# Performance work log

Hardware: AMD Instinct MI355X
Metric: run time of the kernel (lower is better)

## Reference

```python
import jax, jax.numpy as jnp
import numpy as np

B, T, C, U = 256, 512, 256, 64  # batch, time, classes (incl. blank), label length
BLANK = C - 1                   # keras ctc_batch_cost: blank is last class
S = 2 * U + 1                   # extended label length (blanks interleaved)
NEG = -1e30                     # safe log-zero for fp32
EPS = 1e-7                      # keras.backend.epsilon()


def setup_inputs() -> dict:
    key = jax.random.key(0)
    k1, k2 = jax.random.split(key)
    # y_pred are softmax probabilities over time, as fed to ctc_batch_cost
    y_pred = jax.nn.softmax(jax.random.normal(k1, (B, T, C), dtype=jnp.float32), axis=-1)
    # labels exclude the blank index (values in [0, C-2]); all U positions valid
    y_true = jax.random.randint(k2, (B, U), 0, C - 1, dtype=jnp.int32)
    return {"y_true": y_true, "y_pred": y_pred}


def _ctc_loss(y_pred, y_true):
    # keras ctc_batch_cost computes loss on log(y_pred + eps)
    log_probs = jnp.log(y_pred + EPS)                      # [B, T, C]
    # extended label sequence: blank, l1, blank, l2, ..., blank
    ext = jnp.full((B, S), BLANK, dtype=y_true.dtype).at[:, 1::2].set(y_true)
    # gather per-state emission log-probs: lp_ext[b,t,s] = log_probs[b,t,ext[b,s]]
    lp_ext = jnp.take_along_axis(log_probs, ext[:, None, :].astype(jnp.int32), axis=2)  # [B,T,S]
    # skip transition (s-2 -> s) allowed iff ext[s] != blank and ext[s] != ext[s-2]
    ext_m2 = jnp.pad(ext[:, :-2], ((0, 0), (2, 0)), constant_values=-1)
    skip_ok = (ext != BLANK) & (ext != ext_m2)             # [B, S]

    # alpha_0: can start in state 0 (blank) or state 1 (first label)
    alpha0 = (jnp.full((B, S), NEG, dtype=jnp.float32)
              .at[:, 0].set(lp_ext[:, 0, 0])
              .at[:, 1].set(lp_ext[:, 0, 1]))

    def step(alpha, lp_t):
        a1 = jnp.pad(alpha[:, :-1], ((0, 0), (1, 0)), constant_values=NEG)
        a2 = jnp.pad(alpha[:, :-2], ((0, 0), (2, 0)), constant_values=NEG)
        a2 = jnp.where(skip_ok, a2, NEG)
        alpha = jnp.logaddexp(jnp.logaddexp(alpha, a1), a2) + lp_t
        return alpha, None

    lp_time_major = jnp.swapaxes(lp_ext, 0, 1)             # [T, B, S]
    alpha, _ = jax.lax.scan(step, alpha0, lp_time_major[1:])
    # terminate in last blank or last label
    loss = -jnp.logaddexp(alpha[:, -1], alpha[:, -2])      # [B]
    return loss[:, None]                                   # [B, 1] like ctc_batch_cost


def reference(y_true, y_pred):
    return _ctc_loss(y_pred, y_true)
```

## Files before the change

### kernel.cpp

```cpp
#include <hip/hip_runtime.h>


constexpr int B = 256, T = 512, C = 256, U = 64;
constexpr int CH = 16;
constexpr int NBUF = 4;
#define EPSF 1e-7f

__device__ __forceinline__ float dpp_wave_shr1(float x) {
    return __int_as_float(__builtin_amdgcn_update_dpp(
        0, __float_as_int(x), 0x138, 0xf, 0xf, true));
}

#define DPPMAX(ctrl)                                                      \
    {                                                                     \
        float x_ = __int_as_float(__builtin_amdgcn_update_dpp(            \
            0, __float_as_int(m_), (ctrl), 0xf, 0xf, true));              \
        m_ = fmaxf(m_, x_);                                               \
    }

#define RESCALE()                                                         \
    {                                                                     \
        float m_ = fmaxf(fmaxf(a_even, a_odd), a_top);                    \
        DPPMAX(0x111) DPPMAX(0x112) DPPMAX(0x114) DPPMAX(0x118)           \
        DPPMAX(0x142) DPPMAX(0x143)                                       \
        const float mx_ = __int_as_float(                                 \
            __builtin_amdgcn_readlane(__float_as_int(m_), 63));           \
        int e_ = (__float_as_int(mx_) >> 23) & 0xff;                      \
        int k_ = 187 - e_;                                                \
        k_ = k_ > 127 ? 127 : k_;                                         \
        const float s_ = __int_as_float((k_ + 127) << 23);                \
        a_even *= s_; a_odd *= s_; a_top *= s_;                           \
        esum += k_;                                                       \
    }

#define STAGE(cc)                                                          \
    {                                                                      \
        const int cs_ = (cc);                                              \
        float* lbase_ = &rows[cs_ % NBUF][0][0];                           \
        _Pragma("unroll")                                                  \
        for (int i = 0; i < CH; ++i) {                                     \
            int t = 1 + cs_ * CH + i;                                      \
            t = t < T ? t : T - 1;                                         \
            const float* g_ = rowp + (size_t)t * C + (lane << 2);          \
            __builtin_amdgcn_global_load_lds(                              \
                (const __attribute__((address_space(1))) void*)g_,         \
                (__attribute__((address_space(3))) void*)(lbase_ + i * C), \
                16, 0, 0);                                                 \
        }                                                                  \
    }

#define DSR(dst, addr, OS)                                                 \
    asm volatile("ds_read_b32 %0, %1 offset:" OS                           \
                 : "=v"(dst) : "v"(addr));

#define LDS_ISSUE(cc)                                                      \
    {                                                                      \
        const int cr_ = (cc);                                              \
        float(*row_)[C] = rows[cr_ % NBUF];                                \
        const unsigned labA_ = (unsigned)(size_t)                          \
            (__attribute__((address_space(3))) void*)&row_[0][label];      \
        const unsigned blkA_ = (unsigned)(size_t)                          \
            (__attribute__((address_space(3))) void*)&row_[0][C - 1];      \
        DSR(lab[0],  labA_, "0")     DSR(lab[1],  labA_, "1024")           \
        DSR(lab[2],  labA_, "2048")  DSR(lab[3],  labA_, "3072")           \
        DSR(lab[4],  labA_, "4096")  DSR(lab[5],  labA_, "5120")           \
        DSR(lab[6],  labA_, "6144")  DSR(lab[7],  labA_, "7168")           \
        DSR(lab[8],  labA_, "8192")  DSR(lab[9],  labA_, "9216")           \
        DSR(lab[10], labA_, "10240") DSR(lab[11], labA_, "11264")          \
        DSR(lab[12], labA_, "12288") DSR(lab[13], labA_, "13312")          \
        DSR(lab[14], labA_, "14336") DSR(lab[15], labA_, "15360")          \
        DSR(blk[0],  blkA_, "0")     DSR(blk[1],  blkA_, "1024")           \
        DSR(blk[2],  blkA_, "2048")  DSR(blk[3],  blkA_, "3072")           \
        DSR(blk[4],  blkA_, "4096")  DSR(blk[5],  blkA_, "5120")           \
        DSR(blk[6],  blkA_, "6144")  DSR(blk[7],  blkA_, "7168")           \
        DSR(blk[8],  blkA_, "8192")  DSR(blk[9],  blkA_, "9216")           \
        DSR(blk[10], blkA_, "10240") DSR(blk[11], blkA_, "11264")          \
        DSR(blk[12], blkA_, "12288") DSR(blk[13], blkA_, "13312")          \
        DSR(blk[14], blkA_, "14336") DSR(blk[15], blkA_, "15360")          \
    }

#define LGKM_FENCE()                                                       \
    asm volatile("s_waitcnt lgkmcnt(0)" ::: "memory");                     \
    __builtin_amdgcn_sched_barrier(0);

#define COMP_CHUNK(NSTEPS)                                                 \
    {                                                                      \
        _Pragma("unroll")                                                  \
        for (int i = 0; i < (NSTEPS); ++i) {                               \
            const float pb = blk[i] + EPSF;                                \
            const float pl = lab[i] + EPSF;                                \
            const float po = dpp_wave_shr1(a_odd);                         \
            const float skp = skip_ok ? po : 0.f;                          \
            const float ne = (a_even + po) * pb;                           \
            const float no = (a_odd + a_even + skp) * pl;                  \
            const float nt = (a_top + a_odd) * pb;                         \
            a_even = ne; a_odd = no; a_top = nt;                           \
            if (((1 + i) & 7) == 0) RESCALE();                             \
        }                                                                  \
    }

__global__ __launch_bounds__(64) void ctc_kernel(const int* __restrict__ y_true,
                                                 const float* __restrict__ y_pred,
                                                 float* __restrict__ out) {
    __shared__ float rows[NBUF][CH][C];
    const int b = blockIdx.x;
    const int lane = threadIdx.x;
    const int label = y_true[b * U + lane];
    const int label_prev = __shfl_up(label, 1);
    const bool skip_ok = (lane > 0) && (label != label_prev);
    const float* __restrict__ rowp = y_pred + (size_t)b * (T * C);

    float a_even, a_odd, a_top;
    {
        const float pb = rowp[C - 1] + EPSF;
        const float pl = rowp[label] + EPSF;
        a_even = (lane == 0) ? pb : 0.f;
        a_odd  = (lane == 0) ? pl : 0.f;
        a_top  = 0.f;
    }
    int esum = 0;

    STAGE(0);
    STAGE(1);
    STAGE(2);

    float lab[CH], blk[CH];

    for (int c = 0; c < 30; ++c) {
        asm volatile("s_waitcnt vmcnt(32)" ::: "memory");
        __builtin_amdgcn_sched_barrier(0);
        LDS_ISSUE(c);
        __builtin_amdgcn_sched_barrier(0);
        if (c <= 28) STAGE(c + 3);
        LGKM_FENCE();
        COMP_CHUNK(CH);
    }

    {
        asm volatile("s_waitcnt vmcnt(16)" ::: "memory");
        __builtin_amdgcn_sched_barrier(0);
        LDS_ISSUE(30);
        LGKM_FENCE();
        COMP_CHUNK(CH);
    }
    {
        asm volatile("s_waitcnt vmcnt(0)" ::: "memory");
        __builtin_amdgcn_sched_barrier(0);
        LDS_ISSUE(31);
        LGKM_FENCE();
        COMP_CHUNK(CH - 1);
    }

    if (lane == 63)
        out[b] = -logf(a_top + a_odd) + (float)esum * 0.69314718055994531f;
}

extern "C" void kernel_launch(void* const* d_in, const int* in_sizes, int n_in,
                              void* d_out, int out_size, void* d_ws, size_t ws_size,
                              hipStream_t stream) {
    const int* y_true   = (const int*)d_in[0];
    const float* y_pred = (const float*)d_in[1];
    float* out = (float*)d_out;
    hipLaunchKernelGGL(ctc_kernel, dim3(B), dim3(64), 0, stream,
                       y_true, y_pred, out);
}
```

Measured before the change: 193.3 us.

## Split prefetch across four waves with one compute wave and block barriers

The block grows from one wave to four. Each wave now issues global-to-LDS loads for a quarter of the rows in every chunk, while wave 0 alone runs the CTC recurrence. Workgroup barriers, combined with vmcnt waits, coordinate buffer readiness between the waves. The goal is to take load-issue overhead off the serial compute wave. The cost is a barrier per chunk and extra waves competing for issue slots.

```diff
diff --git a/kernel.cpp b/kernel.cpp
--- a/kernel.cpp
+++ b/kernel.cpp
@@ -33,12 +33,13 @@
         esum += k_;                                                       \
     }
 
-#define STAGE(cc)                                                          \
+#define STAGE_W(cc)                                                        \
     {                                                                      \
         const int cs_ = (cc);                                              \
         float* lbase_ = &rows[cs_ % NBUF][0][0];                           \
         _Pragma("unroll")                                                  \
-        for (int i = 0; i < CH; ++i) {                                     \
+        for (int j = 0; j < 4; ++j) {                                      \
+            const int i = rbase + j;                                       \
             int t = 1 + cs_ * CH + i;                                      \
             t = t < T ? t : T - 1;                                         \
             const float* g_ = rowp + (size_t)t * C + (lane << 2);          \
@@ -99,60 +100,68 @@
         }                                                                  \
     }
 
-__global__ __launch_bounds__(64) void ctc_kernel(const int* __restrict__ y_true,
-                                                 const float* __restrict__ y_pred,
-                                                 float* __restrict__ out) {
+__global__ __launch_bounds__(256) void ctc_kernel(const int* __restrict__ y_true,
+                                                  const float* __restrict__ y_pred,
+                                                  float* __restrict__ out) {
     __shared__ float rows[NBUF][CH][C];
     const int b = blockIdx.x;
-    const int lane = threadIdx.x;
-    const int label = y_true[b * U + lane];
-    const int label_prev = __shfl_up(label, 1);
-    const bool skip_ok = (lane > 0) && (label != label_prev);
+    const int tid = threadIdx.x;
+    const int lane = tid & 63;
+    const int wid = tid >> 6;
+    const int rbase = wid << 2;
     const float* __restrict__ rowp = y_pred + (size_t)b * (T * C);
 
-    float a_even, a_odd, a_top;
-    {
+    const int label = y_true[b * U + lane];
+    bool skip_ok = false;
+    float a_even = 0.f, a_odd = 0.f, a_top = 0.f;
+    int esum = 0;
+    float lab[CH], blk[CH];
+
+    if (wid == 0) {
+        const int label_prev = __shfl_up(label, 1);
+        skip_ok = (lane > 0) && (label != label_prev);
         const float pb = rowp[C - 1] + EPSF;
         const float pl = rowp[label] + EPSF;
         a_even = (lane == 0) ? pb : 0.f;
         a_odd  = (lane == 0) ? pl : 0.f;
         a_top  = 0.f;
     }
-    int esum = 0;
+    asm volatile("s_waitcnt vmcnt(0)" ::: "memory");
 
-    STAGE(0);
-    STAGE(1);
-    STAGE(2);
+    STAGE_W(0);
+    STAGE_W(1);
+    STAGE_W(2);
+    asm volatile("s_waitcnt vmcnt(8)" ::: "memory");
+    __builtin_amdgcn_sched_barrier(0);
+    __builtin_amdgcn_s_barrier();
 
-    float lab[CH], blk[CH];
-
-    for (int c = 0; c < 30; ++c) {
-        asm volatile("s_waitcnt vmcnt(32)" ::: "memory");
+    for (int c = 0; c < 29; ++c) {
+        if (wid == 0) { LDS_ISSUE(c); }
         __builtin_amdgcn_sched_barrier(0);
-        LDS_ISSUE(c);
+        STAGE_W(c + 3);
+        if (wid == 0) {
+            LGKM_FENCE();
+            COMP_CHUNK(CH);
+        }
+        asm volatile("s_waitcnt vmcnt(8)" ::: "memory");
         __builtin_amdgcn_sched_barrier(0);
-        if (c <= 28) STAGE(c + 3);
-        LGKM_FENCE();
-        COMP_CHUNK(CH);
+        __builtin_amdgcn_s_barrier();
     }
-
-    {
-        asm volatile("s_waitcnt vmcnt(16)" ::: "memory");
-        __builtin_amdgcn_sched_barrier(0);
-        LDS_ISSUE(30);
-        LGKM_FENCE();
-        COMP_CHUNK(CH);
-    }
-    {
-        asm volatile("s_waitcnt vmcnt(0)" ::: "memory");
-        __builtin_amdgcn_sched_barrier(0);
+    if (wid == 0) { LDS_ISSUE(29); LGKM_FENCE(); COMP_CHUNK(CH); }
+    asm volatile("s_waitcnt vmcnt(4)" ::: "memory");
+    __builtin_amdgcn_sched_barrier(0);
+    __builtin_amdgcn_s_barrier();
+    if (wid == 0) { LDS_ISSUE(30); LGKM_FENCE(); COMP_CHUNK(CH); }
+    asm volatile("s_waitcnt vmcnt(0)" ::: "memory");
+    __builtin_amdgcn_sched_barrier(0);
+    __builtin_amdgcn_s_barrier();
+    if (wid == 0) {
         LDS_ISSUE(31);
         LGKM_FENCE();
         COMP_CHUNK(CH - 1);
+        if (lane == 63)
+            out[b] = -logf(a_top + a_odd) + (float)esum * 0.69314718055994531f;
     }
-
-    if (lane == 63)
-        out[b] = -logf(a_top + a_odd) + (float)esum * 0.69314718055994531f;
 }
 
 extern "C" void kernel_launch(void* const* d_in, const int* in_sizes, int n_in,
@@ -161,6 +170,6 @@
     const int* y_true   = (const int*)d_in[0];
     const float* y_pred = (const float*)d_in[1];
     float* out = (float*)d_out;
-    hipLaunchKernelGGL(ctc_kernel, dim3(B), dim3(64), 0, stream,
+    hipLaunchKernelGGL(ctc_kernel, dim3(B), dim3(256), 0, stream,
                        y_true, y_pred, out);
 }
```

Result: no change. 194.1 us (+0.4%).
